# Performance work log

Hardware: AMD Instinct MI355X
Metric: run time of the kernel (lower is better)

The kernel has to match this reference:

```python
import jax, jax.numpy as jnp
import numpy as np

N_HEADS = 8
N_GROUPS = 32  # GroupNorm groups (normalization(channels) in guided-diffusion)
EPS = 1e-5


def setup_inputs() -> dict:
    key = jax.random.key(0)
    ks = jax.random.split(key, 7)
    b, c, hh, ww = 16, 512, 32, 32
    x = jax.random.normal(ks[0], (b, c, hh, ww), dtype=jnp.float32)
    norm_w = 1.0 + 0.02 * jax.random.normal(ks[1], (c,), dtype=jnp.float32)
    norm_b = 0.02 * jax.random.normal(ks[2], (c,), dtype=jnp.float32)
    # pointwise Conv1d == matmul over channels; note proj_out is zero-initialized
    # in the original, we use random weights so the op is non-trivial.
    qkv_w = jax.random.normal(ks[3], (3 * c, c), dtype=jnp.float32) / np.sqrt(c).astype(np.float32)
    qkv_b = 0.02 * jax.random.normal(ks[4], (3 * c,), dtype=jnp.float32)
    proj_w = jax.random.normal(ks[5], (c, c), dtype=jnp.float32) / np.sqrt(c).astype(np.float32)
    proj_b = 0.02 * jax.random.normal(ks[6], (c,), dtype=jnp.float32)
    return {"x": x, "norm_w": norm_w, "norm_b": norm_b,
            "qkv_w": qkv_w, "qkv_b": qkv_b, "proj_w": proj_w, "proj_b": proj_b}


def reference(x, norm_w, norm_b, qkv_w, qkv_b, proj_w, proj_b):
    b, c, hh, ww = x.shape
    t = hh * ww
    xf = x.reshape(b, c, t)

    # GroupNorm(32, c): normalize over (c//G channels, T) per group
    xg = xf.reshape(b, N_GROUPS, (c // N_GROUPS) * t)
    mu = jnp.mean(xg, axis=-1, keepdims=True)
    var = jnp.var(xg, axis=-1, keepdims=True)
    hn = ((xg - mu) * jax.lax.rsqrt(var + EPS)).reshape(b, c, t)
    hn = hn * norm_w[:, None] + norm_b[:, None]

    # pointwise conv: [b, 3c, t]
    qkv = jnp.einsum('oc,bct->bot', qkv_w, hn) + qkv_b[:, None]

    ch = c // N_HEADS
    qkv = qkv.reshape(b * N_HEADS, 3 * ch, t)
    q, k, v = jnp.split(qkv, 3, axis=1)  # each [b*H, ch, t]
    scale = np.float32(1.0 / np.sqrt(np.sqrt(ch)))
    w = jnp.einsum('bct,bcs->bts', q * scale, k * scale)  # [b*H, t, t]
    w = jax.nn.softmax(w.astype(jnp.float32), axis=-1).astype(qkv.dtype)
    a = jnp.einsum('bts,bcs->bct', w, v).reshape(b, c, t)

    h = jnp.einsum('oc,bct->bot', proj_w, a) + proj_b[:, None]
    return (xf + h).reshape(b, c, hh, ww)
```

## Files before the change

kernel.cpp:

```cpp
#include <hip/hip_runtime.h>

#define TPB 256

typedef __attribute__((ext_vector_type(8))) __bf16 bf16x8;
typedef __attribute__((ext_vector_type(4))) float f32x4;
typedef __attribute__((ext_vector_type(8))) unsigned short u16x8;
typedef __attribute__((ext_vector_type(4))) unsigned short u16x4;
typedef __attribute__((ext_vector_type(4))) unsigned int u32x4;
typedef __attribute__((ext_vector_type(2))) unsigned int u32x2;

typedef __attribute__((address_space(1))) const void gconst_void;
typedef __attribute__((address_space(3))) void lds_void;

__device__ __forceinline__ unsigned short f2bf(float f) {
  unsigned u = __builtin_bit_cast(unsigned, f);
  u += 0x7FFFu + ((u >> 16) & 1u);
  return (unsigned short)(u >> 16);
}

__device__ __forceinline__ float exp2_fast(float x) {
  float r;
  asm("v_exp_f32 %0, %1" : "=v"(r) : "v"(x));
  return r;
}

__device__ __forceinline__ float rcp_fast(float x) {
  float r;
  asm("v_rcp_f32 %0, %1" : "=v"(r) : "v"(x));
  return r;
}

__device__ __forceinline__ unsigned cvt_pk_bf16(float lo, float hi) {
  unsigned r;
  asm("v_cvt_pk_bf16_f32 %0, %1, %2" : "=v"(r) : "v"(lo), "v"(hi));
  return r;
}


__global__ __launch_bounds__(256) void k_gn_fused(const float* __restrict__ x,
                                                  const float* __restrict__ nw,
                                                  const float* __restrict__ nb,
                                                  unsigned short* __restrict__ hnT) {
  int bg = blockIdx.x;
  int b = bg >> 5, g = bg & 31;
  size_t base = (size_t)(b * 512 + g * 16) * 1024;
  const float4* p = reinterpret_cast<const float4*>(x + base);
  float s = 0.f, ss = 0.f;
#pragma unroll
  for (int i = 0; i < 16; ++i) {
    float4 v = p[threadIdx.x + i * 256];
    s += v.x + v.y + v.z + v.w;
    ss += v.x * v.x + v.y * v.y + v.z * v.z + v.w * v.w;
  }
#pragma unroll
  for (int off = 1; off < 64; off <<= 1) {
    s += __shfl_xor(s, off, 64);
    ss += __shfl_xor(ss, off, 64);
  }
  __shared__ float rbuf[4][2];
  __shared__ float stat[2];
  int wave = threadIdx.x >> 6;
  if ((threadIdx.x & 63) == 0) { rbuf[wave][0] = s; rbuf[wave][1] = ss; }
  __syncthreads();
  if (threadIdx.x == 0) {
    float S = 0.f, SS = 0.f;
    for (int i = 0; i < 4; ++i) { S += rbuf[i][0]; SS += rbuf[i][1]; }
    float m = S * (1.f / 16384.f);
    float var = SS * (1.f / 16384.f) - m * m;
    stat[0] = m;
    stat[1] = rsqrtf(var + 1e-5f);
  }
  __syncthreads();
  float mu = stat[0], rinv = stat[1];

  int tid = threadIdx.x;
#pragma unroll
  for (int q = 0; q < 2; ++q) {
    int c0 = g * 16 + q * 8;
    float a[8], bb[8];
#pragma unroll
    for (int cc = 0; cc < 8; ++cc) {
      a[cc] = rinv * nw[c0 + cc];
      bb[cc] = nb[c0 + cc] - mu * a[cc];
    }
    size_t cpart = (size_t)(c0 >> 5) * 512 + (size_t)((c0 >> 3) & 3) * 128;
#pragma unroll
    for (int it = 0; it < 4; ++it) {
      int t = it * 256 + tid;
      u16x8 o;
#pragma unroll
      for (int cc = 0; cc < 8; ++cc) {
        float v = x[base + (size_t)(q * 8 + cc) * 1024 + t];
        o[cc] = f2bf(v * a[cc] + bb[cc]);
      }
      size_t dst = (size_t)b * 524288 + (size_t)(t >> 4) * 8192 + cpart + (t & 15) * 8;
      *reinterpret_cast<u16x8*>(hnT + dst) = o;
    }
  }
}

__global__ void k_f32_to_bf16(const float* __restrict__ src, unsigned short* __restrict__ dst,
                              int n4) {
  int i = blockIdx.x * blockDim.x + threadIdx.x;
  if (i < n4) {
    float4 v = reinterpret_cast<const float4*>(src)[i];
    u16x4 o;
    o[0] = f2bf(v.x); o[1] = f2bf(v.y); o[2] = f2bf(v.z); o[3] = f2bf(v.w);
    reinterpret_cast<u16x4*>(dst)[i] = o;
  }
}

__global__ void k_pack_w(const float* __restrict__ src, unsigned short* __restrict__ dst,
                         int nchunks) {
  int i = blockIdx.x * blockDim.x + threadIdx.x;
  if (i >= nchunks) return;
  int r = i >> 6, k8 = i & 63;
  const float4* s = reinterpret_cast<const float4*>(src + (size_t)r * 512 + k8 * 8);
  float4 v0 = s[0], v1 = s[1];
  u16x8 o;
  o[0] = f2bf(v0.x); o[1] = f2bf(v0.y); o[2] = f2bf(v0.z); o[3] = f2bf(v0.w);
  o[4] = f2bf(v1.x); o[5] = f2bf(v1.y); o[6] = f2bf(v1.z); o[7] = f2bf(v1.w);
  size_t d = (size_t)(r >> 4) * 8192 + (size_t)(k8 >> 2) * 512 + (k8 & 3) * 128 + (r & 15) * 8;
  *reinterpret_cast<u16x8*>(dst + d) = o;
}

#define MFMAS(AF, BF)                                                                     \
  do {                                                                                    \
    _Pragma("unroll") for (int mi = 0; mi < 4; ++mi)                                      \
      _Pragma("unroll") for (int ni = 0; ni < 4; ++ni)                                    \
        acc[mi][ni] =                                                                     \
            __builtin_amdgcn_mfma_f32_16x16x32_bf16(AF[mi], BF[ni], acc[mi][ni], 0, 0, 0);\
  } while (0)

#define LOADT(DA, DB, kb)                                                                 \
  do {                                                                                    \
    _Pragma("unroll") for (int mi = 0; mi < 4; ++mi)                                      \
      DA[mi] = *reinterpret_cast<const bf16x8*>(pA + (size_t)mi * 8192 + (kb) * 512);     \
    _Pragma("unroll") for (int ni = 0; ni < 4; ++ni)                                      \
      DB[ni] = *reinterpret_cast<const bf16x8*>(pB + (size_t)ni * 8192 + (kb) * 512);     \
  } while (0)

__global__ __launch_bounds__(256, 2) void k_qkv_gemm(
    const unsigned short* __restrict__ hnT, const unsigned short* __restrict__ wq,
    const float* __restrict__ qkv_b, unsigned short* __restrict__ Q,
    unsigned short* __restrict__ Kq, unsigned short* __restrict__ Vq) {
  int tid = threadIdx.x;
  int lane = tid & 63, wave = tid >> 6;
  int wm = wave >> 1, wn = wave & 1;
  int g = lane >> 4, li = lane & 15;

  int wg = blockIdx.x;
  int lin = (wg & 7) * 192 + (wg >> 3);
  int bx = lin % 12;
  int tmp = lin / 12;
  int by = tmp & 7;
  int b = tmp >> 3;
  int mbase = by * 128;
  int nbase = bx * 128;

  const unsigned short* pA =
      hnT + (size_t)b * 524288 + (size_t)((mbase + wm * 64) >> 4) * 8192 + lane * 8;
  const unsigned short* pB = wq + (size_t)((nbase + wn * 64) >> 4) * 8192 + lane * 8;

  f32x4 zero = {0.f, 0.f, 0.f, 0.f};
  f32x4 acc[4][4];
#pragma unroll
  for (int mi = 0; mi < 4; ++mi)
#pragma unroll
    for (int ni = 0; ni < 4; ++ni) acc[mi][ni] = zero;

  bf16x8 a0[4], b0[4], a1[4], b1[4];
  LOADT(a0, b0, 0);
#pragma unroll
  for (int kb = 0; kb < 16; kb += 2) {
    if (kb + 1 < 16) LOADT(a1, b1, kb + 1);
    MFMAS(a0, b0);
    if (kb + 2 < 16) LOADT(a0, b0, kb + 2);
    MFMAS(a1, b1);
  }

  const float SCALE = 0.42466090143f;
#pragma unroll
  for (int ni = 0; ni < 4; ++ni) {
    int o = nbase + wn * 64 + ni * 16 + li;
    int h = o / 192;
    int j = o - h * 192;
    int bh = b * 8 + h;
    float bias = qkv_b[o];
#pragma unroll
    for (int mi = 0; mi < 4; ++mi) {
      int t0 = mbase + wm * 64 + mi * 16 + g * 4;
      f32x4 v = acc[mi][ni];
      if (j < 64) {
#pragma unroll
        for (int r = 0; r < 4; ++r)
          Q[((size_t)bh * 1024 + t0 + r) * 64 + j] = f2bf((v[r] + bias) * SCALE);
      } else if (j < 128) {
#pragma unroll
        for (int r = 0; r < 4; ++r)
          Kq[((size_t)bh * 1024 + t0 + r) * 64 + (j - 64)] = f2bf((v[r] + bias) * SCALE);
      } else {
        int ch = j - 128;
        int nj = ch >> 4, liv = ch & 15;
        int stile = t0 >> 6, s0 = t0 & 63;
        int kkc = s0 >> 5, gk = (s0 >> 3) & 3, e0 = s0 & 7;
        u16x4 pv;
#pragma unroll
        for (int r = 0; r < 4; ++r) pv[r] = f2bf(v[r] + bias);
        *reinterpret_cast<u16x4*>(Vq + (size_t)bh * 65536 + (size_t)stile * 4096 +
                                  nj * 1024 + kkc * 512 + gk * 128 + liv * 8 + e0) = pv;
      }
    }
  }
}

__global__ __launch_bounds__(512) void k_attn(
    const unsigned short* __restrict__ Q, const unsigned short* __restrict__ K,
    const unsigned short* __restrict__ Vp, unsigned short* __restrict__ aT) {
  __shared__ unsigned short Kls[2][8192];
  int tid = threadIdx.x;
  int lane = tid & 63, w = tid >> 6;
  int g = lane >> 4, li = lane & 15;

  int wg = blockIdx.x;
  int lin = (wg & 7) * 128 + (wg >> 3);
  int qt = lin & 7;
  int bh = lin >> 3;
  int tq0 = qt * 128;
  int b = bh >> 3, h = bh & 7;

  const unsigned short* Kg = K + (size_t)bh * 1024 * 64;
  const unsigned short* Vb = Vp + (size_t)bh * 65536 + lane * 8;

  bf16x8 qf[2];
  {
    int t = tq0 + w * 16 + li;
    const unsigned short* qp = Q + ((size_t)bh * 1024 + t) * 64 + g * 8;
    qf[0] = *reinterpret_cast<const bf16x8*>(qp);
    qf[1] = *reinterpret_cast<const bf16x8*>(qp + 32);
  }

  const unsigned short* kg[2];
#pragma unroll
  for (int i = 0; i < 2; ++i) {
    int r = w * 16 + i * 8 + (lane >> 3);
    int hh = (r ^ (r >> 2)) & 7;
    int c = ((lane & 7) ^ hh) * 8;
    kg[i] = Kg + (size_t)r * 64 + c;
  }

  int srowK = ((li >> 2) << 3) | (li & 3);

  f32x4 zero = {0.f, 0.f, 0.f, 0.f};
  f32x4 oacc[4];
  f32x4 l_acc = zero;
#pragma unroll
  for (int nj = 0; nj < 4; ++nj) oacc[nj] = zero;
  u32x4 onesw = {0x3F803F80u, 0x3F803F80u, 0x3F803F80u, 0x3F803F80u};
  bf16x8 ones = __builtin_bit_cast(bf16x8, onesw);

#define ISSUE(pp, ph)                                                                    \
  do {                                                                                   \
    _Pragma("unroll") for (int i = 0; i < 2; ++i)                                        \
        __builtin_amdgcn_global_load_lds((gconst_void*)(kg[i] + (size_t)(ph) * 8192),    \
                                         (lds_void*)&Kls[pp][w * 1024 + i * 512], 16, 0, \
                                         0);                                             \
  } while (0)

  ISSUE(0, 0);
  for (int ph = 0; ph < 8; ++ph) {
    asm volatile("s_waitcnt vmcnt(0) lgkmcnt(0)" ::: "memory");
    __builtin_amdgcn_s_barrier();
    asm volatile("" ::: "memory");
    if (ph < 7) ISSUE((ph + 1) & 1, ph + 1);

#pragma unroll
    for (int st = 0; st < 2; ++st) {
      const unsigned short* kbase = &Kls[ph & 1][st * 4096];
      const unsigned short* vt = Vb + (size_t)(ph * 2 + st) * 4096;

      bf16x8 vf0[4];
#pragma unroll
      for (int i = 0; i < 4; ++i) vf0[i] = *reinterpret_cast<const bf16x8*>(vt + i * 512);

      f32x4 sacc[4];
      __builtin_amdgcn_s_setprio(1);
#pragma unroll
      for (int ni = 0; ni < 4; ++ni) {
        int rK = ((ni >> 1) << 5) + ((ni & 1) << 2) + srowK;
        int hs = ((rK ^ (rK >> 2)) & 7) << 4;
        int off0 = ((g << 4)) ^ hs;
        int off1 = (64 + (g << 4)) ^ hs;
        bf16x8 kf0 = *reinterpret_cast<const bf16x8*>(&kbase[rK * 64 + (off0 >> 1)]);
        bf16x8 kf1 = *reinterpret_cast<const bf16x8*>(&kbase[rK * 64 + (off1 >> 1)]);
        f32x4 s0 = __builtin_amdgcn_mfma_f32_16x16x32_bf16(kf0, qf[0], zero, 0, 0, 0);
        sacc[ni] = __builtin_amdgcn_mfma_f32_16x16x32_bf16(kf1, qf[1], s0, 0, 0, 0);
      }
      __builtin_amdgcn_s_setprio(0);

      bf16x8 pfrag[2];
#pragma unroll
      for (int ni = 0; ni < 4; ++ni)
#pragma unroll
        for (int r = 0; r < 4; ++r) sacc[ni][r] = exp2_fast(sacc[ni][r]);
#pragma unroll
      for (int kk = 0; kk < 2; ++kk) {
        u32x4 pw;
        pw[0] = cvt_pk_bf16(sacc[2 * kk][0], sacc[2 * kk][1]);
        pw[1] = cvt_pk_bf16(sacc[2 * kk][2], sacc[2 * kk][3]);
        pw[2] = cvt_pk_bf16(sacc[2 * kk + 1][0], sacc[2 * kk + 1][1]);
        pw[3] = cvt_pk_bf16(sacc[2 * kk + 1][2], sacc[2 * kk + 1][3]);
        pfrag[kk] = __builtin_bit_cast(bf16x8, pw);
      }
      l_acc = __builtin_amdgcn_mfma_f32_16x16x32_bf16(ones, pfrag[0], l_acc, 0, 0, 0);
      l_acc = __builtin_amdgcn_mfma_f32_16x16x32_bf16(ones, pfrag[1], l_acc, 0, 0, 0);

      bf16x8 vf1[4];
#pragma unroll
      for (int i = 0; i < 4; ++i)
        vf1[i] = *reinterpret_cast<const bf16x8*>(vt + (4 + i) * 512);

      __builtin_amdgcn_s_setprio(1);
#pragma unroll
      for (int nj = 0; nj < 2; ++nj) {
        oacc[nj] = __builtin_amdgcn_mfma_f32_16x16x32_bf16(vf0[nj * 2 + 0], pfrag[0], oacc[nj], 0, 0, 0);
        oacc[nj] = __builtin_amdgcn_mfma_f32_16x16x32_bf16(vf0[nj * 2 + 1], pfrag[1], oacc[nj], 0, 0, 0);
      }
#pragma unroll
      for (int nj = 2; nj < 4; ++nj) {
        oacc[nj] = __builtin_amdgcn_mfma_f32_16x16x32_bf16(vf1[(nj - 2) * 2 + 0], pfrag[0], oacc[nj], 0, 0, 0);
        oacc[nj] = __builtin_amdgcn_mfma_f32_16x16x32_bf16(vf1[(nj - 2) * 2 + 1], pfrag[1], oacc[nj], 0, 0, 0);
      }
      __builtin_amdgcn_s_setprio(0);
    }
  }
#undef ISSUE

  {
    float inv = rcp_fast(l_acc[0]);
    int t = tq0 + w * 16 + li;
#pragma unroll
    for (int nj = 0; nj < 4; ++nj) {
      u32x2 ov;
      ov[0] = cvt_pk_bf16(oacc[nj][0] * inv, oacc[nj][1] * inv);
      ov[1] = cvt_pk_bf16(oacc[nj][2] * inv, oacc[nj][3] * inv);
      *reinterpret_cast<u32x2*>(aT + ((size_t)b * 1024 + t) * 512 + h * 64 + nj * 16 + g * 4) = ov;
    }
  }
}

__global__ __launch_bounds__(256) void k_proj_gemm(
    const unsigned short* __restrict__ aT, const unsigned short* __restrict__ wp,
    const float* __restrict__ proj_b, const float* __restrict__ x,
    float* __restrict__ out) {
  __shared__ unsigned short As[2][4096];
  __shared__ unsigned short Bs[2][4096];
  int tid = threadIdx.x;
  int lane = tid & 63, wave = tid >> 6;
  int wm = wave >> 1, wn = wave & 1;
  int g = lane >> 4, li = lane & 15;

  int wg = blockIdx.x;
  int lin = (wg & 7) * 64 + (wg >> 3);
  int bx = lin & 7;
  int tmp = lin >> 3;
  int by = tmp & 3;
  int b = tmp >> 2;
  int mbase = by * 128;
  int nbase = bx * 128;

  const unsigned short* Ag = wp + (size_t)mbase * 512;
  const unsigned short* Bg = aT + (size_t)b * 1024 * 512 + (size_t)nbase * 512;

  int kq = (lane & 3) ^ ((lane >> 3) & 3);
  int rst = wave * 32 + (lane >> 2);
  const char* pA0 = (const char*)Ag + (size_t)rst * 1024 + kq * 16;
  const char* pA1 = pA0 + 16 * 1024;
  const char* pB0 = (const char*)Bg + (size_t)rst * 1024 + kq * 16;
  const char* pB1 = pB0 + 16 * 1024;
  int ldsA0 = wave * 1024, ldsA1 = wave * 1024 + 512;

  int voff = 32 * li + 8 * (g ^ ((li >> 1) & 3));

  f32x4 zero = {0.f, 0.f, 0.f, 0.f};
  f32x4 acc[4][4];
#pragma unroll
  for (int mi = 0; mi < 4; ++mi)
#pragma unroll
    for (int ni = 0; ni < 4; ++ni) acc[mi][ni] = zero;

#define GISSUE(k0, buf)                                                                  \
  do {                                                                                   \
    __builtin_amdgcn_global_load_lds((gconst_void*)(pA0 + (k0) * 2),                     \
                                     (lds_void*)&As[buf][ldsA0], 16, 0, 0);              \
    __builtin_amdgcn_global_load_lds((gconst_void*)(pA1 + (k0) * 2),                     \
                                     (lds_void*)&As[buf][ldsA1], 16, 0, 0);              \
    __builtin_amdgcn_global_load_lds((gconst_void*)(pB0 + (k0) * 2),                     \
                                     (lds_void*)&Bs[buf][ldsA0], 16, 0, 0);              \
    __builtin_amdgcn_global_load_lds((gconst_void*)(pB1 + (k0) * 2),                     \
                                     (lds_void*)&Bs[buf][ldsA1], 16, 0, 0);              \
  } while (0)

  GISSUE(0, 0);
#pragma unroll
  for (int kk = 0; kk < 16; ++kk) {
    asm volatile("s_waitcnt vmcnt(0)" ::: "memory");
    __builtin_amdgcn_s_barrier();
    asm volatile("" ::: "memory");
    if (kk < 15) GISSUE((kk + 1) * 32, (kk + 1) & 1);
    const int cur = kk & 1;
    bf16x8 af[4], bfr[4];
#pragma unroll
    for (int mi = 0; mi < 4; ++mi)
      af[mi] = *reinterpret_cast<const bf16x8*>(&As[cur][wm * 2048 + mi * 512 + voff]);
#pragma unroll
    for (int ni = 0; ni < 4; ++ni)
      bfr[ni] = *reinterpret_cast<const bf16x8*>(&Bs[cur][wn * 2048 + ni * 512 + voff]);
#pragma unroll
    for (int mi = 0; mi < 4; ++mi)
#pragma unroll
      for (int ni = 0; ni < 4; ++ni)
        acc[mi][ni] = __builtin_amdgcn_mfma_f32_16x16x32_bf16(af[mi], bfr[ni], acc[mi][ni], 0, 0, 0);
  }
#undef GISSUE

#pragma unroll
  for (int mi = 0; mi < 4; ++mi) {
#pragma unroll
    for (int ni = 0; ni < 4; ++ni) {
      int t = nbase + wn * 64 + ni * 16 + li;
      f32x4 v = acc[mi][ni];
#pragma unroll
      for (int r = 0; r < 4; ++r) {
        int o = mbase + wm * 64 + mi * 16 + g * 4 + r;
        size_t idx = ((size_t)(b * 512 + o)) * 1024 + t;
        out[idx] = v[r] + proj_b[o] + x[idx];
      }
    }
  }
}

extern "C" void kernel_launch(void* const* d_in, const int* in_sizes, int n_in,
                              void* d_out, int out_size, void* d_ws, size_t ws_size,
                              hipStream_t stream) {
  (void)in_sizes; (void)n_in; (void)out_size; (void)ws_size;
  const float* x = (const float*)d_in[0];
  const float* norm_w = (const float*)d_in[1];
  const float* norm_b = (const float*)d_in[2];
  const float* qkv_w = (const float*)d_in[3];
  const float* qkv_b = (const float*)d_in[4];
  const float* proj_w = (const float*)d_in[5];
  const float* proj_b = (const float*)d_in[6];
  float* out = (float*)d_out;

  char* ws = (char*)d_ws;
  size_t off = 0;
  unsigned short* hnT = (unsigned short*)(ws + off); off += (size_t)16 * 1024 * 512 * 2;
  unsigned short* wqb = (unsigned short*)(ws + off); off += (size_t)1536 * 512 * 2;
  unsigned short* wpb = (unsigned short*)(ws + off); off += (size_t)512 * 512 * 2;
  unsigned short* Qb = (unsigned short*)(ws + off); off += (size_t)128 * 1024 * 64 * 2;
  unsigned short* Kb = (unsigned short*)(ws + off); off += (size_t)128 * 1024 * 64 * 2;
  unsigned short* Vb = (unsigned short*)(ws + off); off += (size_t)128 * 1024 * 64 * 2;

  k_gn_fused<<<512, TPB, 0, stream>>>(x, norm_w, norm_b, hnT);
  k_pack_w<<<(98304 + TPB - 1) / TPB, TPB, 0, stream>>>(qkv_w, wqb, 98304);
  k_f32_to_bf16<<<(262144 / 4 + TPB - 1) / TPB, TPB, 0, stream>>>(proj_w, wpb, 262144 / 4);
  k_qkv_gemm<<<1536, TPB, 0, stream>>>(hnT, wqb, qkv_b, Qb, Kb, Vb);
  k_attn<<<1024, 512, 0, stream>>>(Qb, Kb, Vb, hnT );
  k_proj_gemm<<<512, TPB, 0, stream>>>(hnT, wpb, proj_b, x, out);
}
```

Measured before the change: 128.1 us.

## Shrink attention blocks, interleave two K subtiles, merge weight prep kernels

The attention kernel moves from 512-thread blocks covering 128 queries to 256-thread blocks covering 64 queries, with each wave loading twice as many K rows into LDS. The inner loop is restructured so the QK products for both 64-key subtiles of a phase are issued back to back and their softmax and PV steps are interleaved with V loads, to overlap MFMA, exp and memory latency. The two weight conversion kernels are merged into one launch to save launch overhead. Smaller blocks double K/V global traffic per query and raise register pressure from holding two score and V fragment sets.

```diff
diff --git a/kernel.cpp b/kernel.cpp
--- a/kernel.cpp
+++ b/kernel.cpp
@@ -99,29 +99,25 @@
   }
 }
 
-__global__ void k_f32_to_bf16(const float* __restrict__ src, unsigned short* __restrict__ dst,
-                              int n4) {
+__global__ void k_prep_w(const float* __restrict__ qkv_w, const float* __restrict__ proj_w,
+                         unsigned short* __restrict__ wqb, unsigned short* __restrict__ wpb) {
   int i = blockIdx.x * blockDim.x + threadIdx.x;
-  if (i < n4) {
-    float4 v = reinterpret_cast<const float4*>(src)[i];
+  if (i < 98304) {
+    int r = i >> 6, k8 = i & 63;
+    const float4* s = reinterpret_cast<const float4*>(qkv_w + (size_t)r * 512 + k8 * 8);
+    float4 v0 = s[0], v1 = s[1];
+    u16x8 o;
+    o[0] = f2bf(v0.x); o[1] = f2bf(v0.y); o[2] = f2bf(v0.z); o[3] = f2bf(v0.w);
+    o[4] = f2bf(v1.x); o[5] = f2bf(v1.y); o[6] = f2bf(v1.z); o[7] = f2bf(v1.w);
+    size_t d = (size_t)(r >> 4) * 8192 + (size_t)(k8 >> 2) * 512 + (k8 & 3) * 128 + (r & 15) * 8;
+    *reinterpret_cast<u16x8*>(wqb + d) = o;
+  } else {
+    int j = i - 98304;
+    float4 v = reinterpret_cast<const float4*>(proj_w)[j];
     u16x4 o;
     o[0] = f2bf(v.x); o[1] = f2bf(v.y); o[2] = f2bf(v.z); o[3] = f2bf(v.w);
-    reinterpret_cast<u16x4*>(dst)[i] = o;
-  }
-}
-
-__global__ void k_pack_w(const float* __restrict__ src, unsigned short* __restrict__ dst,
-                         int nchunks) {
-  int i = blockIdx.x * blockDim.x + threadIdx.x;
-  if (i >= nchunks) return;
-  int r = i >> 6, k8 = i & 63;
-  const float4* s = reinterpret_cast<const float4*>(src + (size_t)r * 512 + k8 * 8);
-  float4 v0 = s[0], v1 = s[1];
-  u16x8 o;
-  o[0] = f2bf(v0.x); o[1] = f2bf(v0.y); o[2] = f2bf(v0.z); o[3] = f2bf(v0.w);
-  o[4] = f2bf(v1.x); o[5] = f2bf(v1.y); o[6] = f2bf(v1.z); o[7] = f2bf(v1.w);
-  size_t d = (size_t)(r >> 4) * 8192 + (size_t)(k8 >> 2) * 512 + (k8 & 3) * 128 + (r & 15) * 8;
-  *reinterpret_cast<u16x8*>(dst + d) = o;
+    reinterpret_cast<u16x4*>(wpb)[j] = o;
+  }
 }
 
 #define MFMAS(AF, BF)                                                                     \
@@ -214,7 +210,7 @@
   }
 }
 
-__global__ __launch_bounds__(512) void k_attn(
+__global__ __launch_bounds__(256) void k_attn(
     const unsigned short* __restrict__ Q, const unsigned short* __restrict__ K,
     const unsigned short* __restrict__ Vp, unsigned short* __restrict__ aT) {
   __shared__ unsigned short Kls[2][8192];
@@ -223,10 +219,10 @@
   int g = lane >> 4, li = lane & 15;
 
   int wg = blockIdx.x;
-  int lin = (wg & 7) * 128 + (wg >> 3);
-  int qt = lin & 7;
-  int bh = lin >> 3;
-  int tq0 = qt * 128;
+  int lin = (wg & 7) * 256 + (wg >> 3);
+  int qt = lin & 15;
+  int bh = lin >> 4;
+  int tq0 = qt * 64;
   int b = bh >> 3, h = bh & 7;
 
   const unsigned short* Kg = K + (size_t)bh * 1024 * 64;
@@ -240,10 +236,10 @@
     qf[1] = *reinterpret_cast<const bf16x8*>(qp + 32);
   }
 
-  const unsigned short* kg[2];
-#pragma unroll
-  for (int i = 0; i < 2; ++i) {
-    int r = w * 16 + i * 8 + (lane >> 3);
+  const unsigned short* kg[4];
+#pragma unroll
+  for (int i = 0; i < 4; ++i) {
+    int r = w * 32 + i * 8 + (lane >> 3);
     int hh = (r ^ (r >> 2)) & 7;
     int c = ((lane & 7) ^ hh) * 8;
     kg[i] = Kg + (size_t)r * 64 + c;
@@ -261,10 +257,56 @@
 
 #define ISSUE(pp, ph)                                                                    \
   do {                                                                                   \
-    _Pragma("unroll") for (int i = 0; i < 2; ++i)                                        \
+    _Pragma("unroll") for (int i = 0; i < 4; ++i)                                        \
         __builtin_amdgcn_global_load_lds((gconst_void*)(kg[i] + (size_t)(ph) * 8192),    \
-                                         (lds_void*)&Kls[pp][w * 1024 + i * 512], 16, 0, \
+                                         (lds_void*)&Kls[pp][w * 2048 + i * 512], 16, 0, \
                                          0);                                             \
+  } while (0)
+
+#define QK(kb, sacc)                                                                     \
+  do {                                                                                   \
+    _Pragma("unroll") for (int ni = 0; ni < 4; ++ni) {                                   \
+      int rK = ((ni >> 1) << 5) + ((ni & 1) << 2) + srowK;                               \
+      int hs = ((rK ^ (rK >> 2)) & 7) << 4;                                              \
+      int off0 = (g << 4) ^ hs;                                                          \
+      int off1 = (64 + (g << 4)) ^ hs;                                                   \
+      bf16x8 kf0 = *reinterpret_cast<const bf16x8*>(&(kb)[rK * 64 + (off0 >> 1)]);       \
+      bf16x8 kf1 = *reinterpret_cast<const bf16x8*>(&(kb)[rK * 64 + (off1 >> 1)]);       \
+      f32x4 s0 = __builtin_amdgcn_mfma_f32_16x16x32_bf16(kf0, qf[0], zero, 0, 0, 0);     \
+      sacc[ni] = __builtin_amdgcn_mfma_f32_16x16x32_bf16(kf1, qf[1], s0, 0, 0, 0);       \
+    }                                                                                    \
+  } while (0)
+
+#define SM(sacc, pf)                                                                     \
+  do {                                                                                   \
+    _Pragma("unroll") for (int ni = 0; ni < 4; ++ni)                                     \
+      _Pragma("unroll") for (int r = 0; r < 4; ++r) sacc[ni][r] = exp2_fast(sacc[ni][r]);\
+    _Pragma("unroll") for (int kk = 0; kk < 2; ++kk) {                                   \
+      u32x4 pw;                                                                          \
+      pw[0] = cvt_pk_bf16(sacc[2 * kk][0], sacc[2 * kk][1]);                             \
+      pw[1] = cvt_pk_bf16(sacc[2 * kk][2], sacc[2 * kk][3]);                             \
+      pw[2] = cvt_pk_bf16(sacc[2 * kk + 1][0], sacc[2 * kk + 1][1]);                     \
+      pw[3] = cvt_pk_bf16(sacc[2 * kk + 1][2], sacc[2 * kk + 1][3]);                     \
+      pf[kk] = __builtin_bit_cast(bf16x8, pw);                                           \
+    }                                                                                    \
+    l_acc = __builtin_amdgcn_mfma_f32_16x16x32_bf16(ones, pf[0], l_acc, 0, 0, 0);        \
+    l_acc = __builtin_amdgcn_mfma_f32_16x16x32_bf16(ones, pf[1], l_acc, 0, 0, 0);        \
+  } while (0)
+
+#define PVH(vf, pf, base)                                                                \
+  do {                                                                                   \
+    _Pragma("unroll") for (int j = 0; j < 2; ++j) {                                      \
+      oacc[(base) + j] = __builtin_amdgcn_mfma_f32_16x16x32_bf16(vf[j * 2 + 0], pf[0],   \
+                                                                oacc[(base) + j], 0, 0, 0);\
+      oacc[(base) + j] = __builtin_amdgcn_mfma_f32_16x16x32_bf16(vf[j * 2 + 1], pf[1],   \
+                                                                oacc[(base) + j], 0, 0, 0);\
+    }                                                                                    \
+  } while (0)
+
+#define VLOAD(dst, src, o)                                                               \
+  do {                                                                                   \
+    _Pragma("unroll") for (int i = 0; i < 4; ++i)                                        \
+        dst[i] = *reinterpret_cast<const bf16x8*>((src) + ((o) + i) * 512);              \
   } while (0)
 
   ISSUE(0, 0);
@@ -273,68 +315,33 @@
     __builtin_amdgcn_s_barrier();
     asm volatile("" ::: "memory");
     if (ph < 7) ISSUE((ph + 1) & 1, ph + 1);
-
-#pragma unroll
-    for (int st = 0; st < 2; ++st) {
-      const unsigned short* kbase = &Kls[ph & 1][st * 4096];
-      const unsigned short* vt = Vb + (size_t)(ph * 2 + st) * 4096;
-
-      bf16x8 vf0[4];
-#pragma unroll
-      for (int i = 0; i < 4; ++i) vf0[i] = *reinterpret_cast<const bf16x8*>(vt + i * 512);
-
-      f32x4 sacc[4];
-      __builtin_amdgcn_s_setprio(1);
-#pragma unroll
-      for (int ni = 0; ni < 4; ++ni) {
-        int rK = ((ni >> 1) << 5) + ((ni & 1) << 2) + srowK;
-        int hs = ((rK ^ (rK >> 2)) & 7) << 4;
-        int off0 = ((g << 4)) ^ hs;
-        int off1 = (64 + (g << 4)) ^ hs;
-        bf16x8 kf0 = *reinterpret_cast<const bf16x8*>(&kbase[rK * 64 + (off0 >> 1)]);
-        bf16x8 kf1 = *reinterpret_cast<const bf16x8*>(&kbase[rK * 64 + (off1 >> 1)]);
-        f32x4 s0 = __builtin_amdgcn_mfma_f32_16x16x32_bf16(kf0, qf[0], zero, 0, 0, 0);
-        sacc[ni] = __builtin_amdgcn_mfma_f32_16x16x32_bf16(kf1, qf[1], s0, 0, 0, 0);
-      }
-      __builtin_amdgcn_s_setprio(0);
-
-      bf16x8 pfrag[2];
-#pragma unroll
-      for (int ni = 0; ni < 4; ++ni)
-#pragma unroll
-        for (int r = 0; r < 4; ++r) sacc[ni][r] = exp2_fast(sacc[ni][r]);
-#pragma unroll
-      for (int kk = 0; kk < 2; ++kk) {
-        u32x4 pw;
-        pw[0] = cvt_pk_bf16(sacc[2 * kk][0], sacc[2 * kk][1]);
-        pw[1] = cvt_pk_bf16(sacc[2 * kk][2], sacc[2 * kk][3]);
-        pw[2] = cvt_pk_bf16(sacc[2 * kk + 1][0], sacc[2 * kk + 1][1]);
-        pw[3] = cvt_pk_bf16(sacc[2 * kk + 1][2], sacc[2 * kk + 1][3]);
-        pfrag[kk] = __builtin_bit_cast(bf16x8, pw);
-      }
-      l_acc = __builtin_amdgcn_mfma_f32_16x16x32_bf16(ones, pfrag[0], l_acc, 0, 0, 0);
-      l_acc = __builtin_amdgcn_mfma_f32_16x16x32_bf16(ones, pfrag[1], l_acc, 0, 0, 0);
-
-      bf16x8 vf1[4];
-#pragma unroll
-      for (int i = 0; i < 4; ++i)
-        vf1[i] = *reinterpret_cast<const bf16x8*>(vt + (4 + i) * 512);
-
-      __builtin_amdgcn_s_setprio(1);
-#pragma unroll
-      for (int nj = 0; nj < 2; ++nj) {
-        oacc[nj] = __builtin_amdgcn_mfma_f32_16x16x32_bf16(vf0[nj * 2 + 0], pfrag[0], oacc[nj], 0, 0, 0);
-        oacc[nj] = __builtin_amdgcn_mfma_f32_16x16x32_bf16(vf0[nj * 2 + 1], pfrag[1], oacc[nj], 0, 0, 0);
-      }
-#pragma unroll
-      for (int nj = 2; nj < 4; ++nj) {
-        oacc[nj] = __builtin_amdgcn_mfma_f32_16x16x32_bf16(vf1[(nj - 2) * 2 + 0], pfrag[0], oacc[nj], 0, 0, 0);
-        oacc[nj] = __builtin_amdgcn_mfma_f32_16x16x32_bf16(vf1[(nj - 2) * 2 + 1], pfrag[1], oacc[nj], 0, 0, 0);
-      }
-      __builtin_amdgcn_s_setprio(0);
-    }
+    const unsigned short* kb0 = &Kls[ph & 1][0];
+    const unsigned short* kb1 = &Kls[ph & 1][4096];
+    const unsigned short* vtA = Vb + (size_t)(ph * 2) * 4096;
+    const unsigned short* vtB = vtA + 4096;
+
+    f32x4 saccA[4], saccB[4];
+    bf16x8 vfA0[4], vfA1[4], vfB0[4], vfB1[4];
+    bf16x8 pfA[2], pfB[2];
+
+    VLOAD(vfA0, vtA, 0);
+    QK(kb0, saccA);
+    VLOAD(vfA1, vtA, 4);
+    QK(kb1, saccB);
+    SM(saccA, pfA);
+    VLOAD(vfB0, vtB, 0);
+    PVH(vfA0, pfA, 0);
+    PVH(vfA1, pfA, 2);
+    SM(saccB, pfB);
+    VLOAD(vfB1, vtB, 4);
+    PVH(vfB0, pfB, 0);
+    PVH(vfB1, pfB, 2);
   }
 #undef ISSUE
+#undef QK
+#undef SM
+#undef PVH
+#undef VLOAD
 
   {
     float inv = rcp_fast(l_acc[0]);
@@ -463,9 +470,8 @@
   unsigned short* Vb = (unsigned short*)(ws + off); off += (size_t)128 * 1024 * 64 * 2;
 
   k_gn_fused<<<512, TPB, 0, stream>>>(x, norm_w, norm_b, hnT);
-  k_pack_w<<<(98304 + TPB - 1) / TPB, TPB, 0, stream>>>(qkv_w, wqb, 98304);
-  k_f32_to_bf16<<<(262144 / 4 + TPB - 1) / TPB, TPB, 0, stream>>>(proj_w, wpb, 262144 / 4);
+  k_prep_w<<<640, TPB, 0, stream>>>(qkv_w, proj_w, wqb, wpb);
   k_qkv_gemm<<<1536, TPB, 0, stream>>>(hnT, wqb, qkv_b, Qb, Kb, Vb);
-  k_attn<<<1024, 512, 0, stream>>>(Qb, Kb, Vb, hnT );
+  k_attn<<<2048, TPB, 0, stream>>>(Qb, Kb, Vb, hnT );
   k_proj_gemm<<<512, TPB, 0, stream>>>(hnT, wpb, proj_b, x, out);
 }
```

Result: slower. 133.9 us (+4.5%).
